# Kernel tuning notes

Hardware: AMD Instinct MI355X
Metric: run time of the kernel (lower is better)

Reference implementation:

```python
import jax, jax.numpy as jnp
import numpy as np

H = 128      # num_hidden
C = 384      # num_in
K = 32       # neighbors
N = 10000    # nodes
SCALE = 30.0
EPS = 1e-5

def _gelu(x):
    return jax.nn.gelu(x, approximate=False)  # torch GELU default is exact erf

def _ln(x, g, b):
    m = jnp.mean(x, axis=-1, keepdims=True)
    v = jnp.mean((x - m) ** 2, axis=-1, keepdims=True)
    return (x - m) * jax.lax.rsqrt(v + EPS) * g + b

def setup_inputs() -> dict:
    key = jax.random.key(0)
    ks = jax.random.split(key, 12)
    s = lambda fan_in: 1.0 / np.sqrt(fan_in)
    # weights stored [in, out] (transposed vs torch nn.Linear)
    return {
        "h_V": jax.random.normal(ks[0], (N, H), jnp.float32),
        "h_E": jax.random.normal(ks[1], (N, K, C), jnp.float32),
        "mask_V": jnp.ones((N,), jnp.float32),
        "mask_attend": jnp.ones((N, K), jnp.float32),
        "W1_w": jax.random.uniform(ks[2], (H + C, H), jnp.float32, -s(H + C), s(H + C)),
        "W1_b": jnp.zeros((H,), jnp.float32),
        "W2_w": jax.random.uniform(ks[3], (H, H), jnp.float32, -s(H), s(H)),
        "W2_b": jnp.zeros((H,), jnp.float32),
        "W3_w": jax.random.uniform(ks[4], (H, H), jnp.float32, -s(H), s(H)),
        "W3_b": jnp.zeros((H,), jnp.float32),
        "ln1_g": jnp.ones((H,), jnp.float32),
        "ln1_b": jnp.zeros((H,), jnp.float32),
        "Win_w": jax.random.uniform(ks[5], (H, 4 * H), jnp.float32, -s(H), s(H)),
        "Win_b": jnp.zeros((4 * H,), jnp.float32),
        "Wout_w": jax.random.uniform(ks[6], (4 * H, H), jnp.float32, -s(4 * H), s(4 * H)),
        "Wout_b": jnp.zeros((H,), jnp.float32),
        "ln2_g": jnp.ones((H,), jnp.float32),
        "ln2_b": jnp.zeros((H,), jnp.float32),
    }

def reference(h_V, h_E, mask_V, mask_attend,
              W1_w, W1_b, W2_w, W2_b, W3_w, W3_b,
              ln1_g, ln1_b, Win_w, Win_b, Wout_w, Wout_b, ln2_g, ln2_b):
    # expand node features along neighbor axis and concat with edge features
    h_V_expand = jnp.broadcast_to(h_V[:, None, :], (h_V.shape[0], h_E.shape[1], h_V.shape[1]))
    h_EV = jnp.concatenate([h_V_expand, h_E], axis=-1)          # [N, K, H+C]
    # per-edge 3-layer MLP message
    h = _gelu(h_EV @ W1_w + W1_b)                               # [N, K, H]
    h = _gelu(h @ W2_w + W2_b)
    h_message = h @ W3_w + W3_b
    h_message = mask_attend[..., None] * h_message
    dh = jnp.sum(h_message, axis=-2) / SCALE                    # [N, H]
    h_V = _ln(h_V + dh, ln1_g, ln1_b)
    # position-wise FFN
    dh = _gelu(h_V @ Win_w + Win_b) @ Wout_w + Wout_b
    h_V = _ln(h_V + dh, ln2_g, ln2_b)
    h_V = mask_V[:, None] * h_V
    return h_V
```

## Files before the change

### kernel.cpp

```cpp
#include <hip/hip_runtime.h>
#include <hip/hip_bf16.h>

#define NH 128
#define NC 384
#define NK 32

typedef __attribute__((ext_vector_type(8))) short short8v;
typedef __attribute__((ext_vector_type(4))) float f32x4;

#define MFMA16(a, b, c) __builtin_amdgcn_mfma_f32_16x16x32_bf16((a), (b), (c), 0, 0, 0)

__device__ __forceinline__ ushort f2bf(float x) {
  __hip_bfloat16 h = __float2bfloat16(x);
  ushort u;
  __builtin_memcpy(&u, &h, 2);
  return u;
}

__device__ __forceinline__ short8v ld8(const ushort* p) {
  return *reinterpret_cast<const short8v*>(p);
}
__device__ __forceinline__ void st8(ushort* p, short8v v) {
  *reinterpret_cast<short8v*>(p) = v;
}

__device__ __forceinline__ short8v pack8(float4 a, float4 b) {
  short8v v;
  v[0] = (short)f2bf(a.x); v[1] = (short)f2bf(a.y);
  v[2] = (short)f2bf(a.z); v[3] = (short)f2bf(a.w);
  v[4] = (short)f2bf(b.x); v[5] = (short)f2bf(b.y);
  v[6] = (short)f2bf(b.z); v[7] = (short)f2bf(b.w);
  return v;
}

__device__ __forceinline__ float gelu_f(float x) {
  float x2 = x * x;
  float m = __builtin_fmaf(0.07135481283f, x2, 1.595769122f);
  float e = __expf(-x * m);
  return x * __builtin_amdgcn_rcpf(1.0f + e);
}

__device__ __forceinline__ void lds_barrier() {
  asm volatile("s_waitcnt lgkmcnt(0)" ::: "memory");
  __builtin_amdgcn_sched_barrier(0);
  __builtin_amdgcn_s_barrier();
}

__global__ __launch_bounds__(256) void pack_w(
    const float* __restrict__ W1, const float* __restrict__ W2,
    const float* __restrict__ W3, const float* __restrict__ Win,
    const float* __restrict__ Wout, ushort* __restrict__ ws) {
  int id = blockIdx.x * 256 + threadIdx.x;
  if (id < 65536) {
    int t = id, k = t >> 7, c = t & 127;
    ws[(((k >> 3) << 7) + c) * 8 + (k & 7)] = f2bf(W1[t]);
  } else if (id < 81920) {
    int t = id - 65536, k = t >> 7, c = t & 127;
    ws[65536 + (((k >> 3) << 7) + c) * 8 + (k & 7)] = f2bf(W2[t]);
  } else if (id < 98304) {
    int t = id - 81920, k = t >> 7, c = t & 127;
    ws[81920 + (((k >> 3) << 7) + c) * 8 + (k & 7)] = f2bf(W3[t]);
  } else if (id < 163840) {
    int t = id - 98304, k = t >> 9, c = t & 511;
    ws[98304 + (((k >> 3) << 9) + c) * 8 + (k & 7)] = f2bf(Win[t]);
  } else {
    int t = id - 163840, k = t >> 7, c = t & 127;
    ws[163840 + (((k >> 3) << 7) + c) * 8 + (k & 7)] = f2bf(Wout[t]);
  }
}


__device__ __forceinline__ void issue_chunk(const float* __restrict__ hE,
    int p, int c, int tid, int N, float4& a, float4& b) {
  const int r = tid >> 3;
  const int cb = (tid & 7) * 8;
  const int node = r >> 5, e = r & 31;
  int n = 2 * p + node;
  if (n >= N) n = 0;
  const float* g = hE + ((size_t)n * NK + e) * NC + c * 64 + cb;
  const float4* gp = reinterpret_cast<const float4*>(g);
  a = gp[0];
  b = gp[1];
}

__device__ __forceinline__ void convert_regs(ushort* __restrict__ sC, int tid,
    float4 a, float4 b, bool zz) {
  const int r = tid >> 3, cg = tid & 7;
  short8v v = zz ? (short8v){0, 0, 0, 0, 0, 0, 0, 0} : pack8(a, b);
  st8(sC + r * 64 + ((cg ^ (r & 7)) << 3), v);
}

__device__ __forceinline__ void mfma_chunk64(const ushort* __restrict__ sC,
    const ushort* __restrict__ W1p, int j, f32x4 acc[4],
    int g, int lr, int outcol) {
#pragma unroll
  for (int jj = 0; jj < 2; ++jj) {
    short8v bfr = ld8(W1p + (((16 + j * 8 + jj * 4 + g) * 128) + outcol) * 8);
    const int akg = jj * 4 + g;
#pragma unroll
    for (int rt = 0; rt < 4; ++rt) {
      const int row = rt * 16 + lr;
      short8v af = ld8(sC + row * 64 + ((akg ^ (row & 7)) << 3));
      acc[rt] = MFMA16(af, bfr, acc[rt]);
    }
  }
}

__device__ __forceinline__ void mfma_chunk(const ushort* __restrict__ buf,
    const ushort* __restrict__ Wp, int ktBase, f32x4 acc[4],
    int g, int lr, int outcol) {
#pragma unroll
  for (int j = 0; j < 4; ++j) {
    short8v bfr = ld8(Wp + (((ktBase + j) * 4 + g) * 128 + outcol) * 8);
    const int kcg = j * 4 + g;
#pragma unroll
    for (int rt = 0; rt < 4; ++rt) {
      const int row = rt * 16 + lr;
      short8v af = ld8(buf + row * 128 + ((kcg ^ (row & 15)) << 3));
      acc[rt] = MFMA16(af, bfr, acc[rt]);
    }
  }
}

__device__ __forceinline__ void epi_store(ushort* __restrict__ buf,
    const f32x4 acc[4], const float* __restrict__ bias, int outcol, int g) {
  const float bs = bias[outcol];
#pragma unroll
  for (int rt = 0; rt < 4; ++rt)
#pragma unroll
    for (int i = 0; i < 4; ++i) {
      const int rr = rt * 16 + g * 4 + i;
      buf[rr * 128 + ((((outcol >> 3) ^ (rr & 15)) << 3) | (outcol & 7))] =
          f2bf(gelu_f(acc[rt][i] + bs));
    }
}

__global__ __launch_bounds__(512, 4) void msg3(
    const float* __restrict__ hV, const float* __restrict__ hE,
    const float* __restrict__ mAtt, const ushort* __restrict__ wsu,
    const float* __restrict__ b1, const float* __restrict__ b2,
    const float* __restrict__ b3, const float* __restrict__ g1,
    const float* __restrict__ be1, float* __restrict__ hmidf,
    ushort* __restrict__ hmidb, int N) {
  const ushort* W1p = wsu;
  const ushort* W2p = wsu + 65536;
  const ushort* W3p = wsu + 81920;

  __shared__ ushort sC[2][4096];
  __shared__ ushort sH2[8192];
  __shared__ ushort sHV[256];
  __shared__ float  sDh[256];
  __shared__ float  sRed[16];

  const int tid = threadIdx.x;
  const int w = tid >> 6, lane = tid & 63;
  const int g = lane >> 4, lr = lane & 15;
  const int outcol = (w << 4) + lr;
  const int p = blockIdx.x;
  const bool zz = (2 * p + ((tid >> 3) >> 5)) >= N;

  float4 eA, eB, oA, oB;

  issue_chunk(hE, p, 0, tid, N, eA, eB);
  issue_chunk(hE, p, 1, tid, N, oA, oB);
  if (tid < 32) {
    const int nd = tid >> 4, c8 = tid & 15;
    const int n = 2 * p + nd;
    const int ncl = n < N ? n : 0;
    const float4* hp = reinterpret_cast<const float4*>(hV + (size_t)ncl * NH + c8 * 8);
    st8(sHV + nd * 128 + c8 * 8, pack8(hp[0], hp[1]));
  }
  convert_regs(sC[0], tid, eA, eB, zz);
  lds_barrier();

  f32x4 acc[4];
#pragma unroll
  for (int rt = 0; rt < 4; ++rt) acc[rt] = (f32x4){0.f, 0.f, 0.f, 0.f};

#pragma unroll
  for (int kt = 0; kt < 4; ++kt) {
    short8v bfr = ld8(W1p + ((kt * 4 + g) * 128 + outcol) * 8);
    short8v a0 = ld8(sHV + kt * 32 + g * 8);
    short8v a1 = ld8(sHV + 128 + kt * 32 + g * 8);
    acc[0] = MFMA16(a0, bfr, acc[0]);
    acc[1] = MFMA16(a0, bfr, acc[1]);
    acc[2] = MFMA16(a1, bfr, acc[2]);
    acc[3] = MFMA16(a1, bfr, acc[3]);
  }

  issue_chunk(hE, p, 2, tid, N, eA, eB);
  mfma_chunk64(sC[0], W1p, 0, acc, g, lr, outcol);
  convert_regs(sC[1], tid, oA, oB, zz);
  lds_barrier();
  issue_chunk(hE, p, 3, tid, N, oA, oB);
  mfma_chunk64(sC[1], W1p, 1, acc, g, lr, outcol);
  convert_regs(sC[0], tid, eA, eB, zz);
  lds_barrier();
  issue_chunk(hE, p, 4, tid, N, eA, eB);
  mfma_chunk64(sC[0], W1p, 2, acc, g, lr, outcol);
  convert_regs(sC[1], tid, oA, oB, zz);
  lds_barrier();
  issue_chunk(hE, p, 5, tid, N, oA, oB);
  mfma_chunk64(sC[1], W1p, 3, acc, g, lr, outcol);
  convert_regs(sC[0], tid, eA, eB, zz);
  lds_barrier();
  mfma_chunk64(sC[0], W1p, 4, acc, g, lr, outcol);
  convert_regs(sC[1], tid, oA, oB, zz);
  lds_barrier();
  mfma_chunk64(sC[1], W1p, 5, acc, g, lr, outcol);
  __syncthreads();

  ushort* sH1 = &sC[0][0];
  epi_store(sH1, acc, b1, outcol, g);
  __syncthreads();

#pragma unroll
  for (int rt = 0; rt < 4; ++rt) acc[rt] = (f32x4){0.f, 0.f, 0.f, 0.f};
  mfma_chunk(sH1, W2p, 0, acc, g, lr, outcol);
  epi_store(sH2, acc, b2, outcol, g);
  __syncthreads();

#pragma unroll
  for (int rt = 0; rt < 4; ++rt) acc[rt] = (f32x4){0.f, 0.f, 0.f, 0.f};
  mfma_chunk(sH2, W3p, 0, acc, g, lr, outcol);
  {
    const float bias = b3[outcol];
    float ns0 = 0.f, ns1 = 0.f;
#pragma unroll
    for (int rt = 0; rt < 4; ++rt) {
      const int nd = rt >> 1;
      float s = 0.f;
#pragma unroll
      for (int i = 0; i < 4; ++i) {
        const int e2 = (rt & 1) * 16 + g * 4 + i;
        const float m =
            (2 * p + nd < N) ? mAtt[(size_t)(2 * p + nd) * NK + e2] : 0.f;
        s += (acc[rt][i] + bias) * m;
      }
      s += __shfl_xor(s, 16, 64);
      s += __shfl_xor(s, 32, 64);
      if (rt < 2) ns0 += s; else ns1 += s;
    }
    if (g == 0) { sDh[outcol] = ns0; sDh[128 + outcol] = ns1; }
  }
  __syncthreads();

  float x_ln = 0.f;
  if (tid < 256) {
    const int nd = tid >> 7, i = tid & 127;
    const int gn = 2 * p + nd;
    if (gn < N)
      x_ln = hV[(size_t)gn * NH + i] + sDh[nd * NH + i] * (1.f / 30.f);
    float s = x_ln, qv = x_ln * x_ln;
#pragma unroll
    for (int d = 1; d < 64; d <<= 1) {
      s += __shfl_xor(s, d, 64);
      qv += __shfl_xor(qv, d, 64);
    }
    if (lane == 0) { sRed[w * 2] = s; sRed[w * 2 + 1] = qv; }
  }
  __syncthreads();
  if (tid < 256) {
    const int nd = tid >> 7, i = tid & 127;
    const int gn = 2 * p + nd;
    if (gn < N) {
      const int wb = nd * 2;
      const float s = sRed[wb * 2] + sRed[wb * 2 + 2];
      const float qv = sRed[wb * 2 + 1] + sRed[wb * 2 + 3];
      const float mean = s * (1.f / 128.f);
      const float var = qv * (1.f / 128.f) - mean * mean;
      const float y = (x_ln - mean) * rsqrtf(var + 1e-5f) * g1[i] + be1[i];
      hmidf[(size_t)gn * NH + i] = y;
      hmidb[(size_t)gn * NH + i] = f2bf(y);
    }
  }
}

__global__ __launch_bounds__(256, 4) void ffn_kernel(
    const ushort* __restrict__ wsu, const float* __restrict__ binf,
    const float* __restrict__ boutf, const float* __restrict__ g2,
    const float* __restrict__ be2, const float* __restrict__ maskV,
    const float* __restrict__ hmidf, const ushort* __restrict__ hmidb,
    float* __restrict__ out, int N) {
  const ushort* Winp = wsu + 98304;
  const ushort* Woutp = wsu + 163840;

  __shared__ ushort sX[16 * 128];
  __shared__ ushort sHf[16 * 512];
  __shared__ float  sY[16 * 132];

  const int tid = threadIdx.x;
  const int w = tid >> 6, lane = tid & 63;
  const int g = lane >> 4, lr = lane & 15;
  const int n0 = blockIdx.x * 16;

  {
    const int rr = tid >> 4, c8 = tid & 15;
    const int n = n0 + rr;
    short8v v = {0, 0, 0, 0, 0, 0, 0, 0};
    if (n < N) v = ld8(hmidb + (size_t)n * NH + c8 * 8);
    st8(sX + rr * 128 + ((c8 ^ (rr & 15)) << 3), v);
  }
  __syncthreads();

#pragma unroll
  for (int ct8 = 0; ct8 < 8; ++ct8) {
    const int col = (w * 8 + ct8) * 16 + lr;
    f32x4 a0acc = (f32x4){0.f, 0.f, 0.f, 0.f};
#pragma unroll
    for (int kt = 0; kt < 4; ++kt) {
      short8v b = ld8(Winp + ((kt * 4 + g) * 512 + col) * 8);
      const int kcg = kt * 4 + g;
      const int r0 = lr;
      short8v a0 = ld8(sX + r0 * 128 + ((kcg ^ (r0 & 15)) << 3));
      a0acc = MFMA16(a0, b, a0acc);
    }
    const float bi = binf[col];
#pragma unroll
    for (int i = 0; i < 4; ++i) {
      const int rr = g * 4 + i;
      const float v0 = gelu_f(a0acc[i] + bi);
      sHf[rr * 512 + ((((col >> 3) ^ (rr & 15)) << 3) | (col & 7))] = f2bf(v0);
    }
  }
  __syncthreads();

  f32x4 o0 = (f32x4){0.f, 0.f, 0.f, 0.f}, o1 = o0;
#pragma unroll
  for (int kt = 0; kt < 16; ++kt) {
    const int kcg = kt * 4 + g;
    const int c0 = (2 * w) * 16 + lr, c1 = (2 * w + 1) * 16 + lr;
    short8v b0 = ld8(Woutp + (kcg * 128 + c0) * 8);
    short8v b1 = ld8(Woutp + (kcg * 128 + c1) * 8);
    const int r0 = lr;
    short8v a0 = ld8(sHf + r0 * 512 + ((kcg ^ (r0 & 15)) << 3));
    o0 = MFMA16(a0, b0, o0);
    o1 = MFMA16(a0, b1, o1);
  }
#pragma unroll
  for (int ct = 0; ct < 2; ++ct) {
    const int col = (2 * w + ct) * 16 + lr;
    const float bo = boutf[col];
    const f32x4 oo = ct ? o1 : o0;
#pragma unroll
    for (int i = 0; i < 4; ++i) {
      const int rr = g * 4 + i;
      const int n = n0 + rr;
      const float resid = (n < N) ? hmidf[(size_t)n * NH + col] : 0.f;
      sY[rr * 132 + col] = oo[i] + bo + resid;
    }
  }
  __syncthreads();

  {
    const int rr = tid >> 4, qq = tid & 15;
    const int n = n0 + rr;
    float vals[8];
    float s = 0.f, qs = 0.f;
    const float* yr = sY + rr * 132 + qq * 8;
#pragma unroll
    for (int j = 0; j < 8; ++j) { float x = yr[j]; vals[j] = x; s += x; qs += x * x; }
    s += __shfl_xor(s, 1, 64);  qs += __shfl_xor(qs, 1, 64);
    s += __shfl_xor(s, 2, 64);  qs += __shfl_xor(qs, 2, 64);
    s += __shfl_xor(s, 4, 64);  qs += __shfl_xor(qs, 4, 64);
    s += __shfl_xor(s, 8, 64);  qs += __shfl_xor(qs, 8, 64);
    const float mean = s * (1.f / 128.f);
    const float var = qs * (1.f / 128.f) - mean * mean;
    const float rs = rsqrtf(var + 1e-5f);
    if (n < N) {
      const float mv = maskV[n];
#pragma unroll
      for (int j = 0; j < 8; ++j) {
        const int col = qq * 8 + j;
        out[(size_t)n * NH + col] = ((vals[j] - mean) * rs * g2[col] + be2[col]) * mv;
      }
    }
  }
}

extern "C" void kernel_launch(void* const* d_in, const int* in_sizes, int n_in,
                              void* d_out, int out_size, void* d_ws, size_t ws_size,
                              hipStream_t stream) {
  const float* hV   = (const float*)d_in[0];
  const float* hE   = (const float*)d_in[1];
  const float* mV   = (const float*)d_in[2];
  const float* mAtt = (const float*)d_in[3];
  const float* W1   = (const float*)d_in[4];
  const float* b1   = (const float*)d_in[5];
  const float* W2   = (const float*)d_in[6];
  const float* b2   = (const float*)d_in[7];
  const float* W3   = (const float*)d_in[8];
  const float* b3   = (const float*)d_in[9];
  const float* g1   = (const float*)d_in[10];
  const float* be1  = (const float*)d_in[11];
  const float* Win  = (const float*)d_in[12];
  const float* binf = (const float*)d_in[13];
  const float* Wout = (const float*)d_in[14];
  const float* bout = (const float*)d_in[15];
  const float* g2   = (const float*)d_in[16];
  const float* be2  = (const float*)d_in[17];

  const int N = in_sizes[0] / NH;

  ushort* wsu = (ushort*)d_ws;
  float*  hmidf = (float*)((char*)d_ws + 458752);
  ushort* hmidb = (ushort*)((char*)d_ws + 458752 + (size_t)N * NH * 4);

  pack_w<<<896, 256, 0, stream>>>(W1, W2, W3, Win, Wout, wsu);

  const int pairs = (N + 1) / 2;
  msg3<<<pairs, 512, 0, stream>>>(hV, hE, mAtt, wsu, b1, b2, b3, g1, be1,
                                  hmidf, hmidb, N);
  ffn_kernel<<<(N + 15) / 16, 256, 0, stream>>>(wsu, binf, bout, g2, be2, mV,
                                                hmidf, hmidb, (float*)d_out, N);
  (void)n_in; (void)out_size; (void)ws_size;
}
```

Before: 168.0 us.

## Make message kernel persistent and prefetch next node pair during epilogue

```diff
diff --git a/kernel.cpp b/kernel.cpp
--- a/kernel.cpp
+++ b/kernel.cpp
@@ -135,7 +135,7 @@
     }
 }
 
-__global__ __launch_bounds__(512, 4) void msg3(
+__global__ __launch_bounds__(512, 4) void msg4(
     const float* __restrict__ hV, const float* __restrict__ hE,
     const float* __restrict__ mAtt, const ushort* __restrict__ wsu,
     const float* __restrict__ b1, const float* __restrict__ b2,
@@ -156,123 +156,158 @@
   const int w = tid >> 6, lane = tid & 63;
   const int g = lane >> 4, lr = lane & 15;
   const int outcol = (w << 4) + lr;
-  const int p = blockIdx.x;
-  const bool zz = (2 * p + ((tid >> 3) >> 5)) >= N;
+
+  const int pairs = (N + 1) >> 1;
+  const int stride = gridDim.x;
+  const int bId = blockIdx.x;
+  const int T = (pairs - bId + stride - 1) / stride;
 
   float4 eA, eB, oA, oB;
-
-  issue_chunk(hE, p, 0, tid, N, eA, eB);
-  issue_chunk(hE, p, 1, tid, N, oA, oB);
+  float4 hv0 = (float4){0.f, 0.f, 0.f, 0.f}, hv1 = hv0;
+
+  issue_chunk(hE, bId, 0, tid, N, eA, eB);
+  issue_chunk(hE, bId, 1, tid, N, oA, oB);
   if (tid < 32) {
     const int nd = tid >> 4, c8 = tid & 15;
-    const int n = 2 * p + nd;
+    const int n = 2 * bId + nd;
     const int ncl = n < N ? n : 0;
     const float4* hp = reinterpret_cast<const float4*>(hV + (size_t)ncl * NH + c8 * 8);
-    st8(sHV + nd * 128 + c8 * 8, pack8(hp[0], hp[1]));
-  }
-  convert_regs(sC[0], tid, eA, eB, zz);
-  lds_barrier();
+    float4 h0 = hp[0], h1 = hp[1];
+    if (n >= N) { h0 = (float4){0.f, 0.f, 0.f, 0.f}; h1 = h0; }
+    st8(sHV + nd * 128 + c8 * 8, pack8(h0, h1));
+  }
 
   f32x4 acc[4];
-#pragma unroll
-  for (int rt = 0; rt < 4; ++rt) acc[rt] = (f32x4){0.f, 0.f, 0.f, 0.f};
-
-#pragma unroll
-  for (int kt = 0; kt < 4; ++kt) {
-    short8v bfr = ld8(W1p + ((kt * 4 + g) * 128 + outcol) * 8);
-    short8v a0 = ld8(sHV + kt * 32 + g * 8);
-    short8v a1 = ld8(sHV + 128 + kt * 32 + g * 8);
-    acc[0] = MFMA16(a0, bfr, acc[0]);
-    acc[1] = MFMA16(a0, bfr, acc[1]);
-    acc[2] = MFMA16(a1, bfr, acc[2]);
-    acc[3] = MFMA16(a1, bfr, acc[3]);
-  }
-
-  issue_chunk(hE, p, 2, tid, N, eA, eB);
-  mfma_chunk64(sC[0], W1p, 0, acc, g, lr, outcol);
-  convert_regs(sC[1], tid, oA, oB, zz);
-  lds_barrier();
-  issue_chunk(hE, p, 3, tid, N, oA, oB);
-  mfma_chunk64(sC[1], W1p, 1, acc, g, lr, outcol);
-  convert_regs(sC[0], tid, eA, eB, zz);
-  lds_barrier();
-  issue_chunk(hE, p, 4, tid, N, eA, eB);
-  mfma_chunk64(sC[0], W1p, 2, acc, g, lr, outcol);
-  convert_regs(sC[1], tid, oA, oB, zz);
-  lds_barrier();
-  issue_chunk(hE, p, 5, tid, N, oA, oB);
-  mfma_chunk64(sC[1], W1p, 3, acc, g, lr, outcol);
-  convert_regs(sC[0], tid, eA, eB, zz);
-  lds_barrier();
-  mfma_chunk64(sC[0], W1p, 4, acc, g, lr, outcol);
-  convert_regs(sC[1], tid, oA, oB, zz);
-  lds_barrier();
-  mfma_chunk64(sC[1], W1p, 5, acc, g, lr, outcol);
-  __syncthreads();
-
-  ushort* sH1 = &sC[0][0];
-  epi_store(sH1, acc, b1, outcol, g);
-  __syncthreads();
-
-#pragma unroll
-  for (int rt = 0; rt < 4; ++rt) acc[rt] = (f32x4){0.f, 0.f, 0.f, 0.f};
-  mfma_chunk(sH1, W2p, 0, acc, g, lr, outcol);
-  epi_store(sH2, acc, b2, outcol, g);
-  __syncthreads();
-
-#pragma unroll
-  for (int rt = 0; rt < 4; ++rt) acc[rt] = (f32x4){0.f, 0.f, 0.f, 0.f};
-  mfma_chunk(sH2, W3p, 0, acc, g, lr, outcol);
-  {
-    const float bias = b3[outcol];
-    float ns0 = 0.f, ns1 = 0.f;
-#pragma unroll
-    for (int rt = 0; rt < 4; ++rt) {
-      const int nd = rt >> 1;
-      float s = 0.f;
-#pragma unroll
-      for (int i = 0; i < 4; ++i) {
-        const int e2 = (rt & 1) * 16 + g * 4 + i;
-        const float m =
-            (2 * p + nd < N) ? mAtt[(size_t)(2 * p + nd) * NK + e2] : 0.f;
-        s += (acc[rt][i] + bias) * m;
+
+  for (int t = 0; t < T; ++t) {
+    const int p = bId + t * stride;
+    const bool zz = (2 * p + (tid >> 8)) >= N;
+    const int pn = bId + (t + 1) * stride;
+    const int pnc = pn < pairs ? pn : bId;
+
+    convert_regs(sC[0], tid, eA, eB, zz);
+    lds_barrier();
+
+#pragma unroll
+    for (int rt = 0; rt < 4; ++rt) acc[rt] = (f32x4){0.f, 0.f, 0.f, 0.f};
+
+    issue_chunk(hE, p, 2, tid, N, eA, eB);
+#pragma unroll
+    for (int kt = 0; kt < 4; ++kt) {
+      short8v bfr = ld8(W1p + ((kt * 4 + g) * 128 + outcol) * 8);
+      short8v a0 = ld8(sHV + kt * 32 + g * 8);
+      short8v a1 = ld8(sHV + 128 + kt * 32 + g * 8);
+      acc[0] = MFMA16(a0, bfr, acc[0]);
+      acc[1] = MFMA16(a0, bfr, acc[1]);
+      acc[2] = MFMA16(a1, bfr, acc[2]);
+      acc[3] = MFMA16(a1, bfr, acc[3]);
+    }
+    mfma_chunk64(sC[0], W1p, 0, acc, g, lr, outcol);
+    convert_regs(sC[1], tid, oA, oB, zz);
+    lds_barrier();
+
+    issue_chunk(hE, p, 3, tid, N, oA, oB);
+    mfma_chunk64(sC[1], W1p, 1, acc, g, lr, outcol);
+    convert_regs(sC[0], tid, eA, eB, zz);
+    lds_barrier();
+
+    issue_chunk(hE, p, 4, tid, N, eA, eB);
+    mfma_chunk64(sC[0], W1p, 2, acc, g, lr, outcol);
+    convert_regs(sC[1], tid, oA, oB, zz);
+    lds_barrier();
+
+    issue_chunk(hE, p, 5, tid, N, oA, oB);
+    mfma_chunk64(sC[1], W1p, 3, acc, g, lr, outcol);
+    convert_regs(sC[0], tid, eA, eB, zz);
+    lds_barrier();
+
+    issue_chunk(hE, pnc, 0, tid, N, eA, eB);
+    mfma_chunk64(sC[0], W1p, 4, acc, g, lr, outcol);
+    convert_regs(sC[1], tid, oA, oB, zz);
+    lds_barrier();
+
+    issue_chunk(hE, pnc, 1, tid, N, oA, oB);
+    if (tid < 32) {
+      const int nd = tid >> 4, c8 = tid & 15;
+      const int n = 2 * pnc + nd;
+      const int ncl = n < N ? n : 0;
+      const float4* hp = reinterpret_cast<const float4*>(hV + (size_t)ncl * NH + c8 * 8);
+      hv0 = hp[0]; hv1 = hp[1];
+      if (n >= N) { hv0 = (float4){0.f, 0.f, 0.f, 0.f}; hv1 = hv0; }
+    }
+    mfma_chunk64(sC[1], W1p, 5, acc, g, lr, outcol);
+    lds_barrier();
+
+    ushort* sH1 = &sC[0][0];
+    epi_store(sH1, acc, b1, outcol, g);
+    lds_barrier();
+
+#pragma unroll
+    for (int rt = 0; rt < 4; ++rt) acc[rt] = (f32x4){0.f, 0.f, 0.f, 0.f};
+    mfma_chunk(sH1, W2p, 0, acc, g, lr, outcol);
+    epi_store(sH2, acc, b2, outcol, g);
+    lds_barrier();
+
+#pragma unroll
+    for (int rt = 0; rt < 4; ++rt) acc[rt] = (f32x4){0.f, 0.f, 0.f, 0.f};
+    mfma_chunk(sH2, W3p, 0, acc, g, lr, outcol);
+    {
+      const float bias = b3[outcol];
+      float ns0 = 0.f, ns1 = 0.f;
+#pragma unroll
+      for (int rt = 0; rt < 4; ++rt) {
+        const int nd = rt >> 1;
+        float s = 0.f;
+#pragma unroll
+        for (int i = 0; i < 4; ++i) {
+          const int e2 = (rt & 1) * 16 + g * 4 + i;
+          const float m =
+              (2 * p + nd < N) ? mAtt[(size_t)(2 * p + nd) * NK + e2] : 0.f;
+          s += (acc[rt][i] + bias) * m;
+        }
+        s += __shfl_xor(s, 16, 64);
+        s += __shfl_xor(s, 32, 64);
+        if (rt < 2) ns0 += s; else ns1 += s;
       }
-      s += __shfl_xor(s, 16, 64);
-      s += __shfl_xor(s, 32, 64);
-      if (rt < 2) ns0 += s; else ns1 += s;
-    }
-    if (g == 0) { sDh[outcol] = ns0; sDh[128 + outcol] = ns1; }
-  }
-  __syncthreads();
-
-  float x_ln = 0.f;
-  if (tid < 256) {
-    const int nd = tid >> 7, i = tid & 127;
-    const int gn = 2 * p + nd;
-    if (gn < N)
-      x_ln = hV[(size_t)gn * NH + i] + sDh[nd * NH + i] * (1.f / 30.f);
-    float s = x_ln, qv = x_ln * x_ln;
-#pragma unroll
-    for (int d = 1; d < 64; d <<= 1) {
-      s += __shfl_xor(s, d, 64);
-      qv += __shfl_xor(qv, d, 64);
-    }
-    if (lane == 0) { sRed[w * 2] = s; sRed[w * 2 + 1] = qv; }
-  }
-  __syncthreads();
-  if (tid < 256) {
-    const int nd = tid >> 7, i = tid & 127;
-    const int gn = 2 * p + nd;
-    if (gn < N) {
-      const int wb = nd * 2;
-      const float s = sRed[wb * 2] + sRed[wb * 2 + 2];
-      const float qv = sRed[wb * 2 + 1] + sRed[wb * 2 + 3];
-      const float mean = s * (1.f / 128.f);
-      const float var = qv * (1.f / 128.f) - mean * mean;
-      const float y = (x_ln - mean) * rsqrtf(var + 1e-5f) * g1[i] + be1[i];
-      hmidf[(size_t)gn * NH + i] = y;
-      hmidb[(size_t)gn * NH + i] = f2bf(y);
-    }
+      if (g == 0) { sDh[outcol] = ns0; sDh[128 + outcol] = ns1; }
+    }
+    lds_barrier();
+
+    float x_ln = 0.f;
+    if (tid < 256) {
+      const int nd = tid >> 7, i = tid & 127;
+      const int gn = 2 * p + nd;
+      if (gn < N)
+        x_ln = hV[(size_t)gn * NH + i] + sDh[nd * NH + i] * (1.f / 30.f);
+      float s = x_ln, qv = x_ln * x_ln;
+#pragma unroll
+      for (int d = 1; d < 64; d <<= 1) {
+        s += __shfl_xor(s, d, 64);
+        qv += __shfl_xor(qv, d, 64);
+      }
+      if (lane == 0) { sRed[w * 2] = s; sRed[w * 2 + 1] = qv; }
+    }
+    if (tid < 32) {
+      const int nd = tid >> 4, c8 = tid & 15;
+      st8(sHV + nd * 128 + c8 * 8, pack8(hv0, hv1));
+    }
+    lds_barrier();
+
+    if (tid < 256) {
+      const int nd = tid >> 7, i = tid & 127;
+      const int gn = 2 * p + nd;
+      if (gn < N) {
+        const int wb = nd * 2;
+        const float s = sRed[wb * 2] + sRed[wb * 2 + 2];
+        const float qv = sRed[wb * 2 + 1] + sRed[wb * 2 + 3];
+        const float mean = s * (1.f / 128.f);
+        const float var = qv * (1.f / 128.f) - mean * mean;
+        const float y = (x_ln - mean) * rsqrtf(var + 1e-5f) * g1[i] + be1[i];
+        hmidf[(size_t)gn * NH + i] = y;
+        hmidb[(size_t)gn * NH + i] = f2bf(y);
+      }
+    }
+    lds_barrier();
   }
 }
 
@@ -409,8 +444,9 @@
   pack_w<<<896, 256, 0, stream>>>(W1, W2, W3, Win, Wout, wsu);
 
   const int pairs = (N + 1) / 2;
-  msg3<<<pairs, 512, 0, stream>>>(hV, hE, mAtt, wsu, b1, b2, b3, g1, be1,
-                                  hmidf, hmidb, N);
+  const int grid = pairs < 512 ? pairs : 512;
+  msg4<<<grid, 512, 0, stream>>>(hV, hE, mAtt, wsu, b1, b2, b3, g1, be1,
+                                 hmidf, hmidb, N);
   ffn_kernel<<<(N + 15) / 16, 256, 0, stream>>>(wsu, binf, bout, g2, be2, mV,
                                                 hmidf, hmidb, (float*)d_out, N);
   (void)n_in; (void)out_size; (void)ws_size;
```

After: 270.2 us. 60.8% more time.

## Process one node per 256-thread block with 2x2 MFMA register tiles

Applied to the files above, without the earlier changes.

```diff
diff --git a/kernel.cpp b/kernel.cpp
--- a/kernel.cpp
+++ b/kernel.cpp
@@ -69,188 +69,187 @@
   }
 }
 
-
-__device__ __forceinline__ void issue_chunk(const float* __restrict__ hE,
-    int p, int c, int tid, int N, float4& a, float4& b) {
-  const int r = tid >> 3;
-  const int cb = (tid & 7) * 8;
-  const int node = r >> 5, e = r & 31;
-  int n = 2 * p + node;
-  if (n >= N) n = 0;
-  const float* g = hE + ((size_t)n * NK + e) * NC + c * 64 + cb;
-  const float4* gp = reinterpret_cast<const float4*>(g);
-  a = gp[0];
-  b = gp[1];
-}
-
-__device__ __forceinline__ void convert_regs(ushort* __restrict__ sC, int tid,
-    float4 a, float4 b, bool zz) {
-  const int r = tid >> 3, cg = tid & 7;
-  short8v v = zz ? (short8v){0, 0, 0, 0, 0, 0, 0, 0} : pack8(a, b);
-  st8(sC + r * 64 + ((cg ^ (r & 7)) << 3), v);
-}
-
-__device__ __forceinline__ void mfma_chunk64(const ushort* __restrict__ sC,
-    const ushort* __restrict__ W1p, int j, f32x4 acc[4],
-    int g, int lr, int outcol) {
-#pragma unroll
-  for (int jj = 0; jj < 2; ++jj) {
-    short8v bfr = ld8(W1p + (((16 + j * 8 + jj * 4 + g) * 128) + outcol) * 8);
-    const int akg = jj * 4 + g;
-#pragma unroll
-    for (int rt = 0; rt < 4; ++rt) {
-      const int row = rt * 16 + lr;
-      short8v af = ld8(sC + row * 64 + ((akg ^ (row & 7)) << 3));
-      acc[rt] = MFMA16(af, bfr, acc[rt]);
-    }
-  }
-}
-
-__device__ __forceinline__ void mfma_chunk(const ushort* __restrict__ buf,
-    const ushort* __restrict__ Wp, int ktBase, f32x4 acc[4],
-    int g, int lr, int outcol) {
-#pragma unroll
-  for (int j = 0; j < 4; ++j) {
-    short8v bfr = ld8(Wp + (((ktBase + j) * 4 + g) * 128 + outcol) * 8);
-    const int kcg = j * 4 + g;
-#pragma unroll
-    for (int rt = 0; rt < 4; ++rt) {
-      const int row = rt * 16 + lr;
-      short8v af = ld8(buf + row * 128 + ((kcg ^ (row & 15)) << 3));
-      acc[rt] = MFMA16(af, bfr, acc[rt]);
-    }
-  }
-}
-
-__device__ __forceinline__ void epi_store(ushort* __restrict__ buf,
-    const f32x4 acc[4], const float* __restrict__ bias, int outcol, int g) {
-  const float bs = bias[outcol];
-#pragma unroll
-  for (int rt = 0; rt < 4; ++rt)
-#pragma unroll
-    for (int i = 0; i < 4; ++i) {
-      const int rr = rt * 16 + g * 4 + i;
-      buf[rr * 128 + ((((outcol >> 3) ^ (rr & 15)) << 3) | (outcol & 7))] =
-          f2bf(gelu_f(acc[rt][i] + bs));
-    }
-}
-
-__global__ __launch_bounds__(512, 4) void msg3(
+__global__ __launch_bounds__(256, 4) void msg5(
     const float* __restrict__ hV, const float* __restrict__ hE,
     const float* __restrict__ mAtt, const ushort* __restrict__ wsu,
     const float* __restrict__ b1, const float* __restrict__ b2,
     const float* __restrict__ b3, const float* __restrict__ g1,
     const float* __restrict__ be1, float* __restrict__ hmidf,
-    ushort* __restrict__ hmidb, int N) {
+    ushort* __restrict__ hmidb) {
   const ushort* W1p = wsu;
   const ushort* W2p = wsu + 65536;
   const ushort* W3p = wsu + 81920;
 
-  __shared__ ushort sC[2][4096];
-  __shared__ ushort sH2[8192];
-  __shared__ ushort sHV[256];
-  __shared__ float  sDh[256];
-  __shared__ float  sRed[16];
+  __shared__ ushort sC[2][2048];
+  __shared__ ushort sH2[4096];
+  __shared__ ushort sHV[128];
+  __shared__ float  sDh[128];
+  __shared__ float  sRed[4];
 
   const int tid = threadIdx.x;
   const int w = tid >> 6, lane = tid & 63;
   const int g = lane >> 4, lr = lane & 15;
-  const int outcol = (w << 4) + lr;
-  const int p = blockIdx.x;
-  const bool zz = (2 * p + ((tid >> 3) >> 5)) >= N;
+  const int col0 = (w << 5) + lr;
+  const int col1 = col0 + 16;
+  const int n = blockIdx.x;
+
+  const int srow = tid >> 3, scb = tid & 7;
+  const float* eb = hE + ((size_t)n * NK + srow) * NC + scb * 8;
 
   float4 eA, eB, oA, oB;
 
-  issue_chunk(hE, p, 0, tid, N, eA, eB);
-  issue_chunk(hE, p, 1, tid, N, oA, oB);
-  if (tid < 32) {
-    const int nd = tid >> 4, c8 = tid & 15;
-    const int n = 2 * p + nd;
-    const int ncl = n < N ? n : 0;
-    const float4* hp = reinterpret_cast<const float4*>(hV + (size_t)ncl * NH + c8 * 8);
-    st8(sHV + nd * 128 + c8 * 8, pack8(hp[0], hp[1]));
-  }
-  convert_regs(sC[0], tid, eA, eB, zz);
+  {
+    const float4* p0 = reinterpret_cast<const float4*>(eb);
+    eA = p0[0]; eB = p0[1];
+    const float4* p1 = reinterpret_cast<const float4*>(eb + 64);
+    oA = p1[0]; oB = p1[1];
+  }
+  if (tid < 16) {
+    const float4* hp = reinterpret_cast<const float4*>(hV + (size_t)n * NH + tid * 8);
+    st8(sHV + tid * 8, pack8(hp[0], hp[1]));
+  }
+  st8(&sC[0][srow * 64 + ((scb ^ (srow & 7)) << 3)], pack8(eA, eB));
   lds_barrier();
 
-  f32x4 acc[4];
-#pragma unroll
-  for (int rt = 0; rt < 4; ++rt) acc[rt] = (f32x4){0.f, 0.f, 0.f, 0.f};
+  f32x4 acc[2][2];
+#pragma unroll
+  for (int rt = 0; rt < 2; ++rt)
+#pragma unroll
+    for (int ct = 0; ct < 2; ++ct) acc[rt][ct] = (f32x4){0.f, 0.f, 0.f, 0.f};
 
 #pragma unroll
   for (int kt = 0; kt < 4; ++kt) {
-    short8v bfr = ld8(W1p + ((kt * 4 + g) * 128 + outcol) * 8);
     short8v a0 = ld8(sHV + kt * 32 + g * 8);
-    short8v a1 = ld8(sHV + 128 + kt * 32 + g * 8);
-    acc[0] = MFMA16(a0, bfr, acc[0]);
-    acc[1] = MFMA16(a0, bfr, acc[1]);
-    acc[2] = MFMA16(a1, bfr, acc[2]);
-    acc[3] = MFMA16(a1, bfr, acc[3]);
-  }
-
-  issue_chunk(hE, p, 2, tid, N, eA, eB);
-  mfma_chunk64(sC[0], W1p, 0, acc, g, lr, outcol);
-  convert_regs(sC[1], tid, oA, oB, zz);
-  lds_barrier();
-  issue_chunk(hE, p, 3, tid, N, oA, oB);
-  mfma_chunk64(sC[1], W1p, 1, acc, g, lr, outcol);
-  convert_regs(sC[0], tid, eA, eB, zz);
-  lds_barrier();
-  issue_chunk(hE, p, 4, tid, N, eA, eB);
-  mfma_chunk64(sC[0], W1p, 2, acc, g, lr, outcol);
-  convert_regs(sC[1], tid, oA, oB, zz);
-  lds_barrier();
-  issue_chunk(hE, p, 5, tid, N, oA, oB);
-  mfma_chunk64(sC[1], W1p, 3, acc, g, lr, outcol);
-  convert_regs(sC[0], tid, eA, eB, zz);
-  lds_barrier();
-  mfma_chunk64(sC[0], W1p, 4, acc, g, lr, outcol);
-  convert_regs(sC[1], tid, oA, oB, zz);
-  lds_barrier();
-  mfma_chunk64(sC[1], W1p, 5, acc, g, lr, outcol);
-  __syncthreads();
+    short8v bf0 = ld8(W1p + ((kt * 4 + g) * 128 + col0) * 8);
+    short8v bf1 = ld8(W1p + ((kt * 4 + g) * 128 + col1) * 8);
+    acc[0][0] = MFMA16(a0, bf0, acc[0][0]);
+    acc[0][1] = MFMA16(a0, bf1, acc[0][1]);
+  }
+  acc[1][0] = acc[0][0];
+  acc[1][1] = acc[0][1];
+
+#pragma unroll
+  for (int j = 0; j < 6; ++j) {
+    if (j < 4) {
+      const float4* p = reinterpret_cast<const float4*>(eb + (j + 2) * 64);
+      if ((j & 1) == 0) { eA = p[0]; eB = p[1]; }
+      else              { oA = p[0]; oB = p[1]; }
+    }
+    const ushort* sCb = &sC[j & 1][0];
+#pragma unroll
+    for (int jj = 0; jj < 2; ++jj) {
+      const int akg = jj * 4 + g;
+      short8v bf0 = ld8(W1p + (((16 + j * 8 + jj * 4 + g) * 128) + col0) * 8);
+      short8v bf1 = ld8(W1p + (((16 + j * 8 + jj * 4 + g) * 128) + col1) * 8);
+      const int off = (akg ^ (lr & 7)) << 3;
+      short8v a0 = ld8(sCb + (lr) * 64 + off);
+      short8v a1 = ld8(sCb + (16 + lr) * 64 + off);
+      acc[0][0] = MFMA16(a0, bf0, acc[0][0]);
+      acc[1][0] = MFMA16(a1, bf0, acc[1][0]);
+      acc[0][1] = MFMA16(a0, bf1, acc[0][1]);
+      acc[1][1] = MFMA16(a1, bf1, acc[1][1]);
+    }
+    if (j < 5) {
+      short8v v = ((j & 1) == 0) ? pack8(oA, oB) : pack8(eA, eB);
+      st8(&sC[(j + 1) & 1][srow * 64 + ((scb ^ (srow & 7)) << 3)], v);
+    }
+    lds_barrier();
+  }
 
   ushort* sH1 = &sC[0][0];
-  epi_store(sH1, acc, b1, outcol, g);
-  __syncthreads();
-
-#pragma unroll
-  for (int rt = 0; rt < 4; ++rt) acc[rt] = (f32x4){0.f, 0.f, 0.f, 0.f};
-  mfma_chunk(sH1, W2p, 0, acc, g, lr, outcol);
-  epi_store(sH2, acc, b2, outcol, g);
-  __syncthreads();
-
-#pragma unroll
-  for (int rt = 0; rt < 4; ++rt) acc[rt] = (f32x4){0.f, 0.f, 0.f, 0.f};
-  mfma_chunk(sH2, W3p, 0, acc, g, lr, outcol);
-  {
-    const float bias = b3[outcol];
-    float ns0 = 0.f, ns1 = 0.f;
-#pragma unroll
-    for (int rt = 0; rt < 4; ++rt) {
-      const int nd = rt >> 1;
+  {
+#pragma unroll
+    for (int ct = 0; ct < 2; ++ct) {
+      const int col = ct ? col1 : col0;
+      const float bs = b1[col];
+      const int c8 = col >> 3;
+#pragma unroll
+      for (int rt = 0; rt < 2; ++rt)
+#pragma unroll
+        for (int i = 0; i < 4; ++i) {
+          const int rr = rt * 16 + g * 4 + i;
+          sH1[rr * 128 + (((c8 ^ (rr & 15)) << 3) | (col & 7))] =
+              f2bf(gelu_f(acc[rt][ct][i] + bs));
+        }
+    }
+  }
+  __syncthreads();
+
+#pragma unroll
+  for (int rt = 0; rt < 2; ++rt)
+#pragma unroll
+    for (int ct = 0; ct < 2; ++ct) acc[rt][ct] = (f32x4){0.f, 0.f, 0.f, 0.f};
+#pragma unroll
+  for (int kt = 0; kt < 4; ++kt) {
+    const int kcg = kt * 4 + g;
+    short8v bf0 = ld8(W2p + ((kcg)*128 + col0) * 8);
+    short8v bf1 = ld8(W2p + ((kcg)*128 + col1) * 8);
+    const int off = (kcg ^ lr) << 3;
+    short8v a0 = ld8(sH1 + lr * 128 + off);
+    short8v a1 = ld8(sH1 + (16 + lr) * 128 + off);
+    acc[0][0] = MFMA16(a0, bf0, acc[0][0]);
+    acc[1][0] = MFMA16(a1, bf0, acc[1][0]);
+    acc[0][1] = MFMA16(a0, bf1, acc[0][1]);
+    acc[1][1] = MFMA16(a1, bf1, acc[1][1]);
+  }
+  {
+#pragma unroll
+    for (int ct = 0; ct < 2; ++ct) {
+      const int col = ct ? col1 : col0;
+      const float bs = b2[col];
+      const int c8 = col >> 3;
+#pragma unroll
+      for (int rt = 0; rt < 2; ++rt)
+#pragma unroll
+        for (int i = 0; i < 4; ++i) {
+          const int rr = rt * 16 + g * 4 + i;
+          sH2[rr * 128 + (((c8 ^ (rr & 15)) << 3) | (col & 7))] =
+              f2bf(gelu_f(acc[rt][ct][i] + bs));
+        }
+    }
+  }
+  __syncthreads();
+
+#pragma unroll
+  for (int rt = 0; rt < 2; ++rt)
+#pragma unroll
+    for (int ct = 0; ct < 2; ++ct) acc[rt][ct] = (f32x4){0.f, 0.f, 0.f, 0.f};
+#pragma unroll
+  for (int kt = 0; kt < 4; ++kt) {
+    const int kcg = kt * 4 + g;
+    short8v bf0 = ld8(W3p + ((kcg)*128 + col0) * 8);
+    short8v bf1 = ld8(W3p + ((kcg)*128 + col1) * 8);
+    const int off = (kcg ^ lr) << 3;
+    short8v a0 = ld8(sH2 + lr * 128 + off);
+    short8v a1 = ld8(sH2 + (16 + lr) * 128 + off);
+    acc[0][0] = MFMA16(a0, bf0, acc[0][0]);
+    acc[1][0] = MFMA16(a1, bf0, acc[1][0]);
+    acc[0][1] = MFMA16(a0, bf1, acc[0][1]);
+    acc[1][1] = MFMA16(a1, bf1, acc[1][1]);
+  }
+  {
+#pragma unroll
+    for (int ct = 0; ct < 2; ++ct) {
+      const int col = ct ? col1 : col0;
+      const float bs = b3[col];
       float s = 0.f;
 #pragma unroll
-      for (int i = 0; i < 4; ++i) {
-        const int e2 = (rt & 1) * 16 + g * 4 + i;
-        const float m =
-            (2 * p + nd < N) ? mAtt[(size_t)(2 * p + nd) * NK + e2] : 0.f;
-        s += (acc[rt][i] + bias) * m;
-      }
+      for (int rt = 0; rt < 2; ++rt)
+#pragma unroll
+        for (int i = 0; i < 4; ++i) {
+          const int e = rt * 16 + g * 4 + i;
+          s += (acc[rt][ct][i] + bs) * mAtt[(size_t)n * NK + e];
+        }
       s += __shfl_xor(s, 16, 64);
       s += __shfl_xor(s, 32, 64);
-      if (rt < 2) ns0 += s; else ns1 += s;
-    }
-    if (g == 0) { sDh[outcol] = ns0; sDh[128 + outcol] = ns1; }
+      if (g == 0) sDh[col] = s;
+    }
   }
   __syncthreads();
 
   float x_ln = 0.f;
-  if (tid < 256) {
-    const int nd = tid >> 7, i = tid & 127;
-    const int gn = 2 * p + nd;
-    if (gn < N)
-      x_ln = hV[(size_t)gn * NH + i] + sDh[nd * NH + i] * (1.f / 30.f);
+  if (tid < 128) {
+    x_ln = hV[(size_t)n * NH + tid] + sDh[tid] * (1.f / 30.f);
     float s = x_ln, qv = x_ln * x_ln;
 #pragma unroll
     for (int d = 1; d < 64; d <<= 1) {
@@ -260,19 +259,14 @@
     if (lane == 0) { sRed[w * 2] = s; sRed[w * 2 + 1] = qv; }
   }
   __syncthreads();
-  if (tid < 256) {
-    const int nd = tid >> 7, i = tid & 127;
-    const int gn = 2 * p + nd;
-    if (gn < N) {
-      const int wb = nd * 2;
-      const float s = sRed[wb * 2] + sRed[wb * 2 + 2];
-      const float qv = sRed[wb * 2 + 1] + sRed[wb * 2 + 3];
-      const float mean = s * (1.f / 128.f);
-      const float var = qv * (1.f / 128.f) - mean * mean;
-      const float y = (x_ln - mean) * rsqrtf(var + 1e-5f) * g1[i] + be1[i];
-      hmidf[(size_t)gn * NH + i] = y;
-      hmidb[(size_t)gn * NH + i] = f2bf(y);
-    }
+  if (tid < 128) {
+    const float s = sRed[0] + sRed[2];
+    const float qv = sRed[1] + sRed[3];
+    const float mean = s * (1.f / 128.f);
+    const float var = qv * (1.f / 128.f) - mean * mean;
+    const float y = (x_ln - mean) * rsqrtf(var + 1e-5f) * g1[tid] + be1[tid];
+    hmidf[(size_t)n * NH + tid] = y;
+    hmidb[(size_t)n * NH + tid] = f2bf(y);
   }
 }
 
@@ -408,9 +402,8 @@
 
   pack_w<<<896, 256, 0, stream>>>(W1, W2, W3, Win, Wout, wsu);
 
-  const int pairs = (N + 1) / 2;
-  msg3<<<pairs, 512, 0, stream>>>(hV, hE, mAtt, wsu, b1, b2, b3, g1, be1,
-                                  hmidf, hmidb, N);
+  msg5<<<N, 256, 0, stream>>>(hV, hE, mAtt, wsu, b1, b2, b3, g1, be1,
+                              hmidf, hmidb);
   ffn_kernel<<<(N + 15) / 16, 256, 0, stream>>>(wsu, binf, bout, g2, be2, mV,
                                                 hmidf, hmidb, (float*)d_out, N);
   (void)n_in; (void)out_size; (void)ws_size;
```

New measurement: 211.8 us. 1.26x slower.

## Process 32 nodes per FFN block with 512 threads to reuse weight fragments

Applied to the files above, without the earlier changes.

```diff
diff --git a/kernel.cpp b/kernel.cpp
--- a/kernel.cpp
+++ b/kernel.cpp
@@ -168,7 +168,9 @@
     const int n = 2 * p + nd;
     const int ncl = n < N ? n : 0;
     const float4* hp = reinterpret_cast<const float4*>(hV + (size_t)ncl * NH + c8 * 8);
-    st8(sHV + nd * 128 + c8 * 8, pack8(hp[0], hp[1]));
+    float4 h0 = hp[0], h1 = hp[1];
+    if (n >= N) { h0 = (float4){0.f, 0.f, 0.f, 0.f}; h1 = h0; }
+    st8(sHV + nd * 128 + c8 * 8, pack8(h0, h1));
   }
   convert_regs(sC[0], tid, eA, eB, zz);
   lds_barrier();
@@ -276,7 +278,7 @@
   }
 }
 
-__global__ __launch_bounds__(256, 4) void ffn_kernel(
+__global__ __launch_bounds__(512, 4) void ffn32(
     const ushort* __restrict__ wsu, const float* __restrict__ binf,
     const float* __restrict__ boutf, const float* __restrict__ g2,
     const float* __restrict__ be2, const float* __restrict__ maskV,
@@ -285,14 +287,14 @@
   const ushort* Winp = wsu + 98304;
   const ushort* Woutp = wsu + 163840;
 
-  __shared__ ushort sX[16 * 128];
-  __shared__ ushort sHf[16 * 512];
-  __shared__ float  sY[16 * 132];
+  __shared__ ushort sX[32 * 128];
+  __shared__ ushort sHf[32 * 512];
+  __shared__ float  sY[32 * 132];
 
   const int tid = threadIdx.x;
   const int w = tid >> 6, lane = tid & 63;
   const int g = lane >> 4, lr = lane & 15;
-  const int n0 = blockIdx.x * 16;
+  const int n0 = blockIdx.x * 32;
 
   {
     const int rr = tid >> 4, c8 = tid & 15;
@@ -303,51 +305,66 @@
   }
   __syncthreads();
 
-#pragma unroll
-  for (int ct8 = 0; ct8 < 8; ++ct8) {
-    const int col = (w * 8 + ct8) * 16 + lr;
-    f32x4 a0acc = (f32x4){0.f, 0.f, 0.f, 0.f};
+  {
+    f32x4 accI[4][2];
+#pragma unroll
+    for (int ct = 0; ct < 4; ++ct) {
+      accI[ct][0] = (f32x4){0.f, 0.f, 0.f, 0.f};
+      accI[ct][1] = accI[ct][0];
+    }
 #pragma unroll
     for (int kt = 0; kt < 4; ++kt) {
-      short8v b = ld8(Winp + ((kt * 4 + g) * 512 + col) * 8);
       const int kcg = kt * 4 + g;
-      const int r0 = lr;
-      short8v a0 = ld8(sX + r0 * 128 + ((kcg ^ (r0 & 15)) << 3));
-      a0acc = MFMA16(a0, b, a0acc);
-    }
-    const float bi = binf[col];
-#pragma unroll
-    for (int i = 0; i < 4; ++i) {
-      const int rr = g * 4 + i;
-      const float v0 = gelu_f(a0acc[i] + bi);
-      sHf[rr * 512 + ((((col >> 3) ^ (rr & 15)) << 3) | (col & 7))] = f2bf(v0);
+      short8v a0 = ld8(sX + lr * 128 + ((kcg ^ lr) << 3));
+      short8v a1 = ld8(sX + (16 + lr) * 128 + ((kcg ^ lr) << 3));
+#pragma unroll
+      for (int ct = 0; ct < 4; ++ct) {
+        const int col = (w << 6) + ct * 16 + lr;
+        short8v b = ld8(Winp + (kcg * 512 + col) * 8);
+        accI[ct][0] = MFMA16(a0, b, accI[ct][0]);
+        accI[ct][1] = MFMA16(a1, b, accI[ct][1]);
+      }
+    }
+#pragma unroll
+    for (int ct = 0; ct < 4; ++ct) {
+      const int col = (w << 6) + ct * 16 + lr;
+      const float bi = binf[col];
+      const int c8 = col >> 3;
+#pragma unroll
+      for (int rt = 0; rt < 2; ++rt)
+#pragma unroll
+        for (int i = 0; i < 4; ++i) {
+          const int rr = rt * 16 + g * 4 + i;
+          sHf[rr * 512 + (((c8 ^ (rr & 15)) << 3) | (col & 7))] =
+              f2bf(gelu_f(accI[ct][rt][i] + bi));
+        }
     }
   }
   __syncthreads();
 
   f32x4 o0 = (f32x4){0.f, 0.f, 0.f, 0.f}, o1 = o0;
+  const int ocol = (w << 4) + lr;
 #pragma unroll
   for (int kt = 0; kt < 16; ++kt) {
     const int kcg = kt * 4 + g;
-    const int c0 = (2 * w) * 16 + lr, c1 = (2 * w + 1) * 16 + lr;
-    short8v b0 = ld8(Woutp + (kcg * 128 + c0) * 8);
-    short8v b1 = ld8(Woutp + (kcg * 128 + c1) * 8);
-    const int r0 = lr;
-    short8v a0 = ld8(sHf + r0 * 512 + ((kcg ^ (r0 & 15)) << 3));
-    o0 = MFMA16(a0, b0, o0);
-    o1 = MFMA16(a0, b1, o1);
-  }
-#pragma unroll
-  for (int ct = 0; ct < 2; ++ct) {
-    const int col = (2 * w + ct) * 16 + lr;
-    const float bo = boutf[col];
-    const f32x4 oo = ct ? o1 : o0;
-#pragma unroll
-    for (int i = 0; i < 4; ++i) {
-      const int rr = g * 4 + i;
-      const int n = n0 + rr;
-      const float resid = (n < N) ? hmidf[(size_t)n * NH + col] : 0.f;
-      sY[rr * 132 + col] = oo[i] + bo + resid;
+    short8v b = ld8(Woutp + (kcg * 128 + ocol) * 8);
+    short8v a0 = ld8(sHf + lr * 512 + ((kcg ^ lr) << 3));
+    short8v a1 = ld8(sHf + (16 + lr) * 512 + ((kcg ^ lr) << 3));
+    o0 = MFMA16(a0, b, o0);
+    o1 = MFMA16(a1, b, o1);
+  }
+  {
+    const float bo = boutf[ocol];
+#pragma unroll
+    for (int rt = 0; rt < 2; ++rt) {
+      const f32x4 oo = rt ? o1 : o0;
+#pragma unroll
+      for (int i = 0; i < 4; ++i) {
+        const int rr = rt * 16 + g * 4 + i;
+        const int n = n0 + rr;
+        const float resid = (n < N) ? hmidf[(size_t)n * NH + ocol] : 0.f;
+        sY[rr * 132 + ocol] = oo[i] + bo + resid;
+      }
     }
   }
   __syncthreads();
@@ -411,7 +428,7 @@
   const int pairs = (N + 1) / 2;
   msg3<<<pairs, 512, 0, stream>>>(hV, hE, mAtt, wsu, b1, b2, b3, g1, be1,
                                   hmidf, hmidb, N);
-  ffn_kernel<<<(N + 15) / 16, 256, 0, stream>>>(wsu, binf, bout, g2, be2, mV,
-                                                hmidf, hmidb, (float*)d_out, N);
+  ffn32<<<(N + 31) / 32, 512, 0, stream>>>(wsu, binf, bout, g2, be2, mV,
+                                           hmidf, hmidb, (float*)d_out, N);
   (void)n_in; (void)out_size; (void)ws_size;
 }
```

After: 164.9 us. No clear change (-1.8%).
